# Optimization experiments

Hardware: AMD Instinct MI355X
Metric: run time of the kernel (lower is better)

## Reference

```python
import jax, jax.numpy as jnp
import numpy as np

B, N, D, H, DH, DFF = 2, 2048, 1024, 16, 64, 4096
EPS = 1e-5  # F.layer_norm default


def setup_inputs() -> dict:
    key = jax.random.key(0)
    ks = jax.random.split(key, 8)
    w = lambda k, shape: jax.random.normal(k, shape, dtype=jnp.float32) * 0.02
    # standard rotary frequencies over full head dim (rot_dim = DH)
    inv_freq = 1.0 / (10000.0 ** (jnp.arange(0, DH, 2, dtype=jnp.float32) / DH))
    t = jnp.arange(N, dtype=jnp.float32)
    f = t[:, None] * inv_freq[None, :]          # [N, DH/2]
    freqs = jnp.concatenate([f, f], axis=-1)    # [N, DH]
    return {
        "x": jax.random.normal(ks[0], (B, N, D), dtype=jnp.float32),
        "gamma_pre": jnp.ones((D,), jnp.float32),
        "w_qkv": w(ks[1], (3 * D, D)),
        "w_o": w(ks[2], (D, D)),
        "gamma_ff": jnp.ones((D,), jnp.float32),
        "w_up": w(ks[3], (DFF, D)),
        "b_up": jnp.zeros((DFF,), jnp.float32),
        "w_gate": w(ks[4], (DFF, D)),
        "b_gate": jnp.zeros((DFF,), jnp.float32),
        "w_out": w(ks[5], (D, DFF)),
        "b_out": jnp.zeros((D,), jnp.float32),
        "freqs": freqs,
        "mask": jnp.ones((B, N), dtype=bool),
    }


def _layernorm(x, gamma):
    mu = jnp.mean(x, axis=-1, keepdims=True)
    var = jnp.var(x, axis=-1, keepdims=True)
    return (x - mu) * jax.lax.rsqrt(var + EPS) * gamma


def _rotate_half(x):
    x1, x2 = jnp.split(x, 2, axis=-1)
    return jnp.concatenate([-x2, x1], axis=-1)


def _rope(t, freqs):
    # rot_dim == DH so nothing is left unrotated
    return t * jnp.cos(freqs) + _rotate_half(t) * jnp.sin(freqs)


def reference(x, gamma_pre, w_qkv, w_o, gamma_ff, w_up, b_up, w_gate, b_gate,
              w_out, b_out, freqs, mask):
    b, n, d = x.shape
    # ---- self-attention branch (pre-norm) ----
    h = _layernorm(x, gamma_pre)
    qkv = h @ w_qkv.T                                   # [b, n, 3d]
    q, k, v = jnp.split(qkv, 3, axis=-1)
    to_heads = lambda t: t.reshape(b, n, H, DH).transpose(0, 2, 1, 3)  # b h n d
    q, k, v = to_heads(q), to_heads(k), to_heads(v)
    q = _rope(q, freqs)
    k = _rope(k, freqs)
    scale = 1.0 / np.sqrt(DH).astype(np.float32)
    dots = jnp.einsum('bhid,bhjd->bhij', q, k) * scale  # [b, H, n, n]
    neg = -jnp.finfo(dots.dtype).max
    dots = jnp.where(mask[:, None, None, :], dots, neg)        # key padding mask
    causal = jnp.triu(jnp.ones((n, n), dtype=bool), 1)
    dots = jnp.where(causal, neg, dots)
    attn = jax.nn.softmax(dots.astype(jnp.float32), axis=-1).astype(dots.dtype)
    o = jnp.einsum('bhij,bhjd->bhid', attn, v)
    o = o.transpose(0, 2, 1, 3).reshape(b, n, d) @ w_o.T
    o = jnp.where(mask[..., None], o, 0.0)
    x = x + o
    # ---- GLU feed-forward branch (pre-norm) ----
    h2 = _layernorm(x, gamma_ff)
    up = h2 @ w_up.T + b_up
    gate = h2 @ w_gate.T + b_gate
    ff = (up * jax.nn.silu(gate)) @ w_out.T + b_out
    return x + ff
```

## Files before the change

### kernel.cpp

```cpp
#include <hip/hip_runtime.h>
#include <stdint.h>


#define B_ 2
#define N_ 2048
#define D_ 1024
#define H_ 16
#define DFF_ 4096
#define ROWS_ (B_*N_)

typedef unsigned short u16;
typedef short short4_ __attribute__((ext_vector_type(4)));
typedef short short8 __attribute__((ext_vector_type(8)));
typedef float float4_ __attribute__((ext_vector_type(4)));

#define NEGBIG (-1e30f)
#define QSCALE 0.1803368801111204f

__device__ __forceinline__ float b2f(u16 u) {
  union { unsigned u; float f; } c; c.u = ((unsigned)u) << 16; return c.f;
}
__device__ __forceinline__ u16 f2b(float f) {
  union { float f; unsigned u; } c; c.f = f;
  unsigned x = c.u;
  x += 0x7fffu + ((x >> 16) & 1u);
  return (u16)(x >> 16);
}

__device__ __forceinline__ void gl_lds16(const u16* g, u16* l) {
  __builtin_amdgcn_global_load_lds(
      (const __attribute__((address_space(1))) unsigned int*)g,
      (__attribute__((address_space(3))) unsigned int*)l, 16, 0, 0);
}

__global__ __launch_bounds__(256) void cvt_all(const float* __restrict__ s_qkv,
                                               const float* __restrict__ s_o,
                                               const float* __restrict__ s_up,
                                               const float* __restrict__ s_gate,
                                               const float* __restrict__ s_out,
                                               u16* __restrict__ d_qkv,
                                               u16* __restrict__ d_o,
                                               u16* __restrict__ d_up,
                                               u16* __restrict__ d_gate,
                                               u16* __restrict__ d_out_) {
  int c = blockIdx.x * 256 + threadIdx.x;
  const float* src; u16* dst; int off;
  if (c < 393216)       { src = s_qkv;  dst = d_qkv;  off = c; }
  else if (c < 524288)  { src = s_o;    dst = d_o;    off = c - 393216; }
  else if (c < 1048576) { src = s_up;   dst = d_up;   off = c - 524288; }
  else if (c < 1572864) { src = s_gate; dst = d_gate; off = c - 1048576; }
  else                  { src = s_out;  dst = d_out_; off = c - 1572864; }
  int i = off * 8;
  float4_ v0 = *(const float4_*)(src + i);
  float4_ v1 = *(const float4_*)(src + i + 4);
  short8 pk;
#pragma unroll
  for (int e = 0; e < 4; e++) { pk[e] = (short)f2b(v0[e]); pk[4 + e] = (short)f2b(v1[e]); }
  *(short8*)(dst + i) = pk;
}

__global__ __launch_bounds__(256) void ln_kernel(const float* __restrict__ xin,
                                                 const float* __restrict__ gamma,
                                                 u16* __restrict__ out) {
  int row = blockIdx.x, t = threadIdx.x;
  float4_ v = *(const float4_*)(xin + (size_t)row * D_ + t * 4);
  float s = 0.f, ss = 0.f;
#pragma unroll
  for (int i = 0; i < 4; i++) { s += v[i]; ss += v[i] * v[i]; }
#pragma unroll
  for (int off = 1; off < 64; off <<= 1) {
    s  += __shfl_xor(s, off, 64);
    ss += __shfl_xor(ss, off, 64);
  }
  __shared__ float red[8];
  if ((t & 63) == 0) { red[t >> 6] = s; red[4 + (t >> 6)] = ss; }
  __syncthreads();
  s  = red[0] + red[1] + red[2] + red[3];
  ss = red[4] + red[5] + red[6] + red[7];
  float mu  = s * (1.f / D_);
  float var = ss * (1.f / D_) - mu * mu;
  float rs  = rsqrtf(var + 1e-5f);
#pragma unroll
  for (int i = 0; i < 4; i++)
    out[(size_t)row * D_ + t * 4 + i] = f2b((v[i] - mu) * rs * gamma[t * 4 + i]);
}

__global__ __launch_bounds__(256) void combine_ln(const u16* p0,
                                                  const u16* __restrict__ p1,
                                                  const float* __restrict__ resid,
                                                  const float* __restrict__ gamma,
                                                  float* __restrict__ x1,
                                                  u16* h2out) {
  int row = blockIdx.x, t = threadIdx.x;
  size_t base = (size_t)row * D_ + t * 4;
  short4_ a = *(const short4_*)(p0 + base);
  short4_ b = *(const short4_*)(p1 + base);
  float4_ rv = *(const float4_*)(resid + base);
  float4_ v;
  float s = 0.f, ss = 0.f;
#pragma unroll
  for (int i = 0; i < 4; i++) {
    v[i] = b2f((u16)a[i]) + b2f((u16)b[i]) + rv[i];
    s += v[i]; ss += v[i] * v[i];
  }
  *(float4_*)(x1 + base) = v;
#pragma unroll
  for (int off = 1; off < 64; off <<= 1) {
    s  += __shfl_xor(s, off, 64);
    ss += __shfl_xor(ss, off, 64);
  }
  __shared__ float red[8];
  if ((t & 63) == 0) { red[t >> 6] = s; red[4 + (t >> 6)] = ss; }
  __syncthreads();
  s  = red[0] + red[1] + red[2] + red[3];
  ss = red[4] + red[5] + red[6] + red[7];
  float mu  = s * (1.f / D_);
  float var = ss * (1.f / D_) - mu * mu;
  float rs  = rsqrtf(var + 1e-5f);
#pragma unroll
  for (int i = 0; i < 4; i++)
    h2out[base + i] = f2b((v[i] - mu) * rs * gamma[t * 4 + i]);
}

template <int MODE>
__device__ __forceinline__ void gemm_epilogue(float4_ (&acc)[4][4], void* Cout,
                                              const float* bias, const void* extra,
                                              int mbase, int nbase, int N,
                                              int wr, int wc, int quad, int l16) {
#pragma unroll
  for (int i = 0; i < 4; i++) {
#pragma unroll
    for (int r = 0; r < 4; r++) {
      int row = mbase + wr * 64 + i * 16 + quad * 4 + r;
#pragma unroll
      for (int j = 0; j < 4; j++) {
        int col = nbase + wc * 64 + j * 16 + l16;
        size_t idx = (size_t)row * N + col;
        float v = acc[i][j][r];
        if (MODE == 0) {
          ((u16*)Cout)[idx] = f2b(v);
        } else if (MODE == 1) {
          ((u16*)Cout)[idx] = f2b(v + bias[col]);
        } else if (MODE == 2) {
          ((float*)Cout)[idx] = v + ((const float*)extra)[idx];
        } else if (MODE == 3) {
          float gate = v + bias[col];
          float sig = 1.f / (1.f + expf(-gate));
          float upv = b2f(((const u16*)extra)[idx]);
          ((u16*)Cout)[idx] = f2b(upv * gate * sig);
        } else {
          ((float*)Cout)[idx] = v + bias[col] + ((const float*)extra)[idx];
        }
      }
    }
  }
}

__device__ __forceinline__ void gemm_core64(const u16* A, const u16* W,
                                            float4_ (&acc)[4][4], u16* sA, u16* sW,
                                            int mbase, int nbase, int K,
                                            int klo, int khi,
                                            int wave, int lane, int wr, int wc,
                                            int quad, int l16) {
  int colb = ((lane & 3) ^ ((lane >> 3) & 3)) << 3;
  int qs8  = (quad ^ ((l16 >> 1) & 3)) * 8;
  for (int k0 = klo; k0 < khi; k0 += 64) {
    __syncthreads();
#pragma unroll
    for (int hh = 0; hh < 2; hh++) {
      int kh = k0 + hh * 32;
#pragma unroll
      for (int it = 0; it < 2; it++) {
        int c = wave * 128 + it * 64 + lane;
        int row = c >> 2;
        gl_lds16(A + (size_t)(mbase + row) * K + kh + colb,
                 sA + hh * 4096 + (size_t)(wave * 128 + it * 64) * 8);
        gl_lds16(W + (size_t)(nbase + row) * K + kh + colb,
                 sW + hh * 4096 + (size_t)(wave * 128 + it * 64) * 8);
      }
    }
    __syncthreads();
#pragma unroll
    for (int hh = 0; hh < 2; hh++) {
      const u16* sAp = sA + hh * 4096;
      const u16* sWp = sW + hh * 4096;
      short8 af[4], bf[4];
#pragma unroll
      for (int i = 0; i < 4; i++)
        af[i] = *(const short8*)(sAp + (wr * 64 + i * 16 + l16) * 32 + qs8);
#pragma unroll
      for (int j = 0; j < 4; j++)
        bf[j] = *(const short8*)(sWp + (wc * 64 + j * 16 + l16) * 32 + qs8);
#pragma unroll
      for (int i = 0; i < 4; i++)
#pragma unroll
        for (int j = 0; j < 4; j++)
          acc[i][j] = __builtin_amdgcn_mfma_f32_16x16x32_bf16(af[i], bf[j], acc[i][j], 0, 0, 0);
    }
  }
}

__global__ __launch_bounds__(256) void gemm_bb(const u16* __restrict__ A,
                                               const u16* __restrict__ W,
                                               u16* __restrict__ C,
                                               int M, int N, int K) {
  __shared__ __align__(16) u16 sA[2][128 * 32];
  __shared__ __align__(16) u16 sW[2][128 * 32];
  int t = threadIdx.x;
  int mbase = blockIdx.y * 128, nbase = blockIdx.x * 128;
  int wave = t >> 6, lane = t & 63;
  int wr = wave >> 1, wc = wave & 1;
  int quad = lane >> 4, l16 = lane & 15;

  float4_ z4 = {0.f, 0.f, 0.f, 0.f};
  float4_ acc[4][4];
#pragma unroll
  for (int i = 0; i < 4; i++)
#pragma unroll
    for (int j = 0; j < 4; j++) acc[i][j] = z4;

  gemm_core64(A, W, acc, &sA[0][0], &sW[0][0], mbase, nbase, K,
              0, K, wave, lane, wr, wc, quad, l16);

#pragma unroll
  for (int i = 0; i < 4; i++)
#pragma unroll
    for (int r = 0; r < 4; r++) {
      int row = mbase + wr * 64 + i * 16 + quad * 4 + r;
#pragma unroll
      for (int j = 0; j < 4; j++) {
        int col = nbase + wc * 64 + j * 16 + l16;
        C[(size_t)row * N + col] = f2b(acc[i][j][r]);
      }
    }
}

__global__ __launch_bounds__(256) void gemm_bb_split(const u16* __restrict__ A,
                                                     const u16* __restrict__ W,
                                                     u16* __restrict__ p0,
                                                     u16* __restrict__ p1,
                                                     int M, int N, int K) {
  __shared__ __align__(16) u16 sA[2][128 * 32];
  __shared__ __align__(16) u16 sW[2][128 * 32];
  int t = threadIdx.x;
  int mbase = blockIdx.y * 128, nbase = blockIdx.x * 128;
  int z = blockIdx.z;
  int wave = t >> 6, lane = t & 63;
  int wr = wave >> 1, wc = wave & 1;
  int quad = lane >> 4, l16 = lane & 15;
  int Kh = K >> 1;

  float4_ z4 = {0.f, 0.f, 0.f, 0.f};
  float4_ acc[4][4];
#pragma unroll
  for (int i = 0; i < 4; i++)
#pragma unroll
    for (int j = 0; j < 4; j++) acc[i][j] = z4;

  gemm_core64(A, W, acc, &sA[0][0], &sW[0][0], mbase, nbase, K,
              z * Kh, z * Kh + Kh, wave, lane, wr, wc, quad, l16);

  u16* P = z ? p1 : p0;
#pragma unroll
  for (int i = 0; i < 4; i++)
#pragma unroll
    for (int r = 0; r < 4; r++) {
      int row = mbase + wr * 64 + i * 16 + quad * 4 + r;
#pragma unroll
      for (int j = 0; j < 4; j++) {
        int col = nbase + wc * 64 + j * 16 + l16;
        P[(size_t)row * N + col] = f2b(acc[i][j][r]);
      }
    }
}

__device__ __forceinline__ void glu8_stageA(const u16* A, u16* aslot, int mbase,
                                            int kk, int wave, int lane, int colb) {
  int rw = wave * 16 + (lane >> 2);
#pragma unroll
  for (int it = 0; it < 2; it++) {
    int row = it * 128 + rw;
    gl_lds16(A + (size_t)(mbase + row) * 1024 + kk * 32 + colb,
             aslot + it * 4096 + wave * 512);
  }
}
__device__ __forceinline__ void glu8_stageB(const u16* Wu, const u16* Wg, u16* bslot,
                                            int nbase, int kk, int wave, int lane,
                                            int colb) {
  int rw = wave * 16 + (lane >> 2);
  size_t go = (size_t)(nbase + rw) * 1024 + kk * 32 + colb;
  gl_lds16(Wu + go, bslot + wave * 512);
  gl_lds16(Wg + go, bslot + 4096 + wave * 512);
}

__global__ __launch_bounds__(512) void gemm_glu8(const u16* __restrict__ A,
                                                 const u16* __restrict__ Wu,
                                                 const u16* __restrict__ Wg,
                                                 const float* __restrict__ bu,
                                                 const float* __restrict__ bg,
                                                 u16* __restrict__ G) {
  __shared__ __align__(16) u16 ring[4][16384];
  const int NT = 32;
  int t_ = threadIdx.x, wave = t_ >> 6, lane = t_ & 63;
  int wr = wave >> 2, wc = wave & 3;
  int quad = lane >> 4, l16 = lane & 15;
  int mbase = blockIdx.y * 256, nbase = blockIdx.x * 128;
  int colb = ((lane & 3) ^ ((lane >> 3) & 3)) << 3;
  int qs8  = (quad ^ ((l16 >> 1) & 3)) * 8;

  float4_ z4 = {0.f, 0.f, 0.f, 0.f};
  float4_ acc[8][4];
#pragma unroll
  for (int i = 0; i < 8; i++)
#pragma unroll
    for (int j = 0; j < 4; j++) acc[i][j] = z4;

#pragma unroll
  for (int kk = 0; kk < 3; kk++) {
    glu8_stageA(A, ring[kk], mbase, kk, wave, lane, colb);
    glu8_stageB(Wu, Wg, ring[kk] + 8192, nbase, kk, wave, lane, colb);
  }

  for (int t = 0; t < NT; t++) {
    if (t < NT - 2)       asm volatile("s_waitcnt vmcnt(8)" ::: "memory");
    else if (t == NT - 2) asm volatile("s_waitcnt vmcnt(4)" ::: "memory");
    else                  asm volatile("s_waitcnt vmcnt(0)" ::: "memory");
    __builtin_amdgcn_s_barrier();
    asm volatile("" ::: "memory");

    const u16* as = ring[t & 3];
    const u16* bs = as + 8192;
    bool prefetch = (t + 3 < NT);
    int kk = t + 3;

    if (prefetch) glu8_stageA(A, ring[kk & 3], mbase, kk, wave, lane, colb);
    short8 af[4], bf[4];
#pragma unroll
    for (int i = 0; i < 4; i++)
      af[i] = *(const short8*)(as + (wr * 128 + i * 16 + l16) * 32 + qs8);
#pragma unroll
    for (int j = 0; j < 4; j++)
      bf[j] = *(const short8*)(bs + (wc * 64 + j * 16 + l16) * 32 + qs8);
    __builtin_amdgcn_s_setprio(1);
#pragma unroll
    for (int i = 0; i < 4; i++)
#pragma unroll
      for (int j = 0; j < 4; j++)
        acc[i][j] = __builtin_amdgcn_mfma_f32_16x16x32_bf16(af[i], bf[j], acc[i][j], 0, 0, 0);
    __builtin_amdgcn_s_setprio(0);
    __builtin_amdgcn_s_barrier();
    asm volatile("" ::: "memory");

    if (prefetch) glu8_stageB(Wu, Wg, ring[kk & 3] + 8192, nbase, kk, wave, lane, colb);
    short8 ag[4];
#pragma unroll
    for (int i = 0; i < 4; i++)
      ag[i] = *(const short8*)(as + (wr * 128 + (4 + i) * 16 + l16) * 32 + qs8);
    __builtin_amdgcn_s_setprio(1);
#pragma unroll
    for (int i = 0; i < 4; i++)
#pragma unroll
      for (int j = 0; j < 4; j++)
        acc[4 + i][j] = __builtin_amdgcn_mfma_f32_16x16x32_bf16(ag[i], bf[j], acc[4 + i][j], 0, 0, 0);
    __builtin_amdgcn_s_setprio(0);
  }

  __syncthreads();
  u16* ex = &ring[0][0];
  if (wc >= 2) {
    int cc = (wc - 2) * 64;
#pragma unroll
    for (int i = 0; i < 8; i++)
#pragma unroll
      for (int r = 0; r < 4; r++) {
        int row = wr * 128 + i * 16 + quad * 4 + r;
#pragma unroll
        for (int j = 0; j < 4; j++) {
          int col = cc + j * 16 + l16;
          float gv = acc[i][j][r] + bg[nbase + col];
          float sig = 1.f / (1.f + expf(-gv));
          ex[row * 128 + col] = f2b(gv * sig);
        }
      }
  }
  __syncthreads();
  if (wc < 2) {
    int cc = wc * 64;
#pragma unroll
    for (int i = 0; i < 8; i++)
#pragma unroll
      for (int r = 0; r < 4; r++) {
        int row = wr * 128 + i * 16 + quad * 4 + r;
#pragma unroll
        for (int j = 0; j < 4; j++) {
          int col = cc + j * 16 + l16;
          float uv = acc[i][j][r] + bu[nbase + col];
          G[(size_t)(mbase + row) * DFF_ + nbase + col] =
              f2b(uv * b2f(ex[row * 128 + col]));
        }
      }
  }
}

__global__ __launch_bounds__(256) void split_combine(const u16* __restrict__ p0,
                                                     const u16* __restrict__ p1,
                                                     const float* __restrict__ bias,
                                                     const float* __restrict__ resid,
                                                     float* __restrict__ out, int N) {
  int idx = (blockIdx.x * 256 + threadIdx.x) * 8;
  int col = idx & (N - 1);
  short8 a = *(const short8*)(p0 + idx);
  short8 b = *(const short8*)(p1 + idx);
  float4_ r0 = *(const float4_*)(resid + idx);
  float4_ r1 = *(const float4_*)(resid + idx + 4);
  float4_ o0, o1;
#pragma unroll
  for (int e = 0; e < 4; e++) {
    float bb0 = bias ? bias[col + e] : 0.f;
    float bb1 = bias ? bias[col + 4 + e] : 0.f;
    o0[e] = b2f((u16)a[e]) + b2f((u16)b[e]) + bb0 + r0[e];
    o1[e] = b2f((u16)a[4 + e]) + b2f((u16)b[4 + e]) + bb1 + r1[e];
  }
  *(float4_*)(out + idx) = o0;
  *(float4_*)(out + idx + 4) = o1;
}

template <int MODE>
__global__ __launch_bounds__(256) void gemm_nt(const u16* __restrict__ A,
                                               const float* __restrict__ W,
                                               void* Cout,
                                               const float* __restrict__ bias,
                                               const void* extra,
                                               int M, int N, int K) {
  __shared__ __align__(16) u16 sA[128 * 32];
  __shared__ __align__(16) u16 sW[128 * 32];
  int t = threadIdx.x;
  int mbase = blockIdx.y * 128, nbase = blockIdx.x * 128;
  int wave = t >> 6, lane = t & 63;
  int wr = wave >> 1, wc = wave & 1;
  int quad = lane >> 4, l16 = lane & 15;

  float4_ z4 = {0.f, 0.f, 0.f, 0.f};
  float4_ acc[4][4];
#pragma unroll
  for (int i = 0; i < 4; i++)
#pragma unroll
    for (int j = 0; j < 4; j++) acc[i][j] = z4;

  for (int k0 = 0; k0 < K; k0 += 32) {
    __syncthreads();
#pragma unroll
    for (int it = 0; it < 2; it++) {
      int c = t + 256 * it;
      int row = c >> 2, col = (c & 3) << 3;
      ((short8*)sA)[c] = *(const short8*)(A + (size_t)(mbase + row) * K + k0 + col);
      const float* wp = W + (size_t)(nbase + row) * K + k0 + col;
      float4_ w0 = *(const float4_*)wp;
      float4_ w1 = *(const float4_*)(wp + 4);
      short8 pk;
#pragma unroll
      for (int e = 0; e < 4; e++) { pk[e] = (short)f2b(w0[e]); pk[4 + e] = (short)f2b(w1[e]); }
      ((short8*)sW)[c] = pk;
    }
    __syncthreads();
    short8 af[4], bf[4];
#pragma unroll
    for (int i = 0; i < 4; i++)
      af[i] = *(const short8*)(sA + (wr * 64 + i * 16 + l16) * 32 + quad * 8);
#pragma unroll
    for (int j = 0; j < 4; j++)
      bf[j] = *(const short8*)(sW + (wc * 64 + j * 16 + l16) * 32 + quad * 8);
#pragma unroll
    for (int i = 0; i < 4; i++)
#pragma unroll
      for (int j = 0; j < 4; j++)
        acc[i][j] = __builtin_amdgcn_mfma_f32_16x16x32_bf16(af[i], bf[j], acc[i][j], 0, 0, 0);
  }
  gemm_epilogue<MODE>(acc, Cout, bias, extra, mbase, nbase, N, wr, wc, quad, l16);
}

template <int SPLIT>
__global__ __launch_bounds__(256) void rope_kernel(const u16* __restrict__ q0,
                                                   const u16* __restrict__ q1,
                                                   const float* __restrict__ freqs,
                                                   u16* __restrict__ qr,
                                                   u16* __restrict__ kr,
                                                   u16* __restrict__ vt) {
  int idx = blockIdx.x * 256 + threadIdx.x;
  int d2 = idx & 31;
  int h  = (idx >> 5) & 15;
  int n  = (idx >> 9) & 2047;
  int b  = idx >> 20;
  float f = freqs[n * 64 + d2];
  float c = cosf(f), s = sinf(f);
  size_t base = (size_t)(b * N_ + n) * 3072;
  int hd = h * 64 + d2;
#define LD(o) (SPLIT ? (b2f(q0[base + (o)]) + b2f(q1[base + (o)])) : b2f(q0[base + (o)]))
  float v_q1 = LD(hd),        v_q2 = LD(hd + 32);
  float v_k1 = LD(1024 + hd), v_k2 = LD(1024 + hd + 32);
  float v_v1 = LD(2048 + hd), v_v2 = LD(2048 + hd + 32);
#undef LD
  size_t ro = ((size_t)(b * H_ + h) * N_ + n) * 64 + d2;
  qr[ro]      = f2b((v_q1 * c - v_q2 * s) * QSCALE);
  qr[ro + 32] = f2b((v_q2 * c + v_q1 * s) * QSCALE);
  kr[ro]      = f2b(v_k1 * c - v_k2 * s);
  kr[ro + 32] = f2b(v_k2 * c + v_k1 * s);
  size_t vo = ((size_t)(b * H_ + h) * 64 + d2) * N_ + n;
  vt[vo]           = f2b(v_v1);
  vt[vo + 32 * N_] = f2b(v_v2);
}

#define LP 72
#define NSPLIT 4
__global__ __launch_bounds__(256) void attn_kernel(const u16* __restrict__ qr,
                                                   const u16* __restrict__ kr,
                                                   const u16* __restrict__ vt,
                                                   u16* __restrict__ opart,
                                                   float* __restrict__ mlp) {
  __shared__ __align__(16) u16 sK[64 * LP];
  __shared__ __align__(16) u16 sV[64 * LP];
  __shared__ __align__(16) u16 sP[4][16 * LP];
  int qp = blockIdx.x, bh = blockIdx.y, sp = blockIdx.z;
  int t = threadIdx.x, wave = t >> 6, lane = t & 63;
  int quad = lane >> 4, l16 = lane & 15;
  const u16* qptr = qr + (size_t)bh * N_ * 64;
  const u16* kp = kr + (size_t)bh * N_ * 64;
  const u16* vp = vt + (size_t)bh * 64 * N_;
  float4_ z4 = {0.f, 0.f, 0.f, 0.f};
  short8 onesv;
#pragma unroll
  for (int e = 0; e < 8; e++) onesv[e] = (short)0x3F80;

  for (int qsel = 0; qsel < 2; qsel++) {
    int qt = qsel ? (N_ / 64 - 1 - qp) : qp;
    int qbase = qt * 64;
    int ntiles = qt + 1;
    int ktlo = (ntiles * sp) / NSPLIT, kthi = (ntiles * (sp + 1)) / NSPLIT;

    short8 aq[2];
    int qrow = qbase + wave * 16 + l16;
#pragma unroll
    for (int kk = 0; kk < 2; kk++)
      aq[kk] = *(const short8*)(qptr + (size_t)qrow * 64 + kk * 32 + quad * 8);

    float4_ o[4] = {z4, z4, z4, z4};
    float m_r[4] = {NEGBIG, NEGBIG, NEGBIG, NEGBIG};
    float l_r[4] = {0.f, 0.f, 0.f, 0.f};

    for (int kt = ktlo; kt < kthi; kt++) {
      __syncthreads();
      {
        const u16* src = kp + (size_t)kt * 64 * 64;
#pragma unroll
        for (int it = 0; it < 2; it++) {
          int c = t + 256 * it;
          int row = c >> 3, seg = c & 7;
          *(short8*)(sK + row * LP + seg * 8) = *(const short8*)(src + c * 8);
          *(short8*)(sV + row * LP + seg * 8) =
              *(const short8*)(vp + (size_t)row * N_ + kt * 64 + seg * 8);
        }
      }
      __syncthreads();

      float4_ sf[4];
#pragma unroll
      for (int j = 0; j < 4; j++) {
        short8 bk0 = *(const short8*)(sK + (j * 16 + l16) * LP + quad * 8);
        short8 bk1 = *(const short8*)(sK + (j * 16 + l16) * LP + 32 + quad * 8);
        float4_ acc = z4;
        acc = __builtin_amdgcn_mfma_f32_16x16x32_bf16(aq[0], bk0, acc, 0, 0, 0);
        acc = __builtin_amdgcn_mfma_f32_16x16x32_bf16(aq[1], bk1, acc, 0, 0, 0);
        sf[j] = acc;
      }
      if (kt == qt) {
#pragma unroll
        for (int j = 0; j < 4; j++)
#pragma unroll
          for (int r = 0; r < 4; r++) {
            int ig = qbase + wave * 16 + quad * 4 + r;
            int jg = kt * 64 + j * 16 + l16;
            if (jg > ig) sf[j][r] = NEGBIG;
          }
      }

      float alpha_r[4], mt_r[4];
#pragma unroll
      for (int r = 0; r < 4; r++)
        mt_r[r] = fmaxf(fmaxf(sf[0][r], sf[1][r]), fmaxf(sf[2][r], sf[3][r]));
      bool need = (mt_r[0] > m_r[0] + 8.f) || (mt_r[1] > m_r[1] + 8.f) ||
                  (mt_r[2] > m_r[2] + 8.f) || (mt_r[3] > m_r[3] + 8.f);
      if (__any(need)) {
#pragma unroll
        for (int r = 0; r < 4; r++) {
          float mt = mt_r[r];
#pragma unroll
          for (int off = 1; off < 16; off <<= 1) mt = fmaxf(mt, __shfl_xor(mt, off, 64));
          float mn = fmaxf(m_r[r], mt);
          alpha_r[r] = exp2f(m_r[r] - mn);
          m_r[r] = mn;
#pragma unroll
          for (int jo = 0; jo < 4; jo++) o[jo][r] *= alpha_r[r];
        }
      } else {
#pragma unroll
        for (int r = 0; r < 4; r++) alpha_r[r] = 1.f;
      }
#pragma unroll
      for (int r = 0; r < 4; r++)
#pragma unroll
        for (int j = 0; j < 4; j++) sf[j][r] = exp2f(sf[j][r] - m_r[r]);

      u16* sPw = sP[wave];
#pragma unroll
      for (int j = 0; j < 4; j++)
#pragma unroll
        for (int r = 0; r < 4; r++)
          sPw[(quad * 4 + r) * LP + j * 16 + l16] = f2b(sf[j][r]);
      short8 ap[2];
#pragma unroll
      for (int kk = 0; kk < 2; kk++)
        ap[kk] = *(const short8*)(sPw + l16 * LP + kk * 32 + quad * 8);

      float4_ ls = z4;
      ls = __builtin_amdgcn_mfma_f32_16x16x32_bf16(ap[0], onesv, ls, 0, 0, 0);
      ls = __builtin_amdgcn_mfma_f32_16x16x32_bf16(ap[1], onesv, ls, 0, 0, 0);
#pragma unroll
      for (int r = 0; r < 4; r++) l_r[r] = l_r[r] * alpha_r[r] + ls[r];

#pragma unroll
      for (int jo = 0; jo < 4; jo++)
#pragma unroll
        for (int kk = 0; kk < 2; kk++) {
          short8 bv = *(const short8*)(sV + (jo * 16 + l16) * LP + kk * 32 + quad * 8);
          o[jo] = __builtin_amdgcn_mfma_f32_16x16x32_bf16(ap[kk], bv, o[jo], 0, 0, 0);
        }
    }

#pragma unroll
    for (int r = 0; r < 4; r++) {
      int n = qbase + wave * 16 + quad * 4 + r;
      size_t row = (size_t)bh * N_ + n;
      if (l16 == 0) {
        mlp[2 * (sp * (size_t)65536 + row)]     = m_r[r];
        mlp[2 * (sp * (size_t)65536 + row) + 1] = l_r[r];
      }
#pragma unroll
      for (int jo = 0; jo < 4; jo++)
        opart[sp * (size_t)4194304 + row * 64 + jo * 16 + l16] = f2b(o[jo][r]);
    }
  }
}

__global__ __launch_bounds__(256) void attn_combine(const u16* __restrict__ opart,
                                                    const float* __restrict__ mlp,
                                                    u16* __restrict__ obuf) {
  int idx = blockIdx.x * 256 + threadIdx.x;
  int row = idx >> 3, seg = idx & 7;
  float mm[NSPLIT], ll[NSPLIT];
  float mmax = NEGBIG;
#pragma unroll
  for (int s = 0; s < NSPLIT; s++) {
    mm[s] = mlp[2 * (s * (size_t)65536 + row)];
    ll[s] = mlp[2 * (s * (size_t)65536 + row) + 1];
    mmax = fmaxf(mmax, mm[s]);
  }
  float w[NSPLIT], lsum = 0.f;
#pragma unroll
  for (int s = 0; s < NSPLIT; s++) { w[s] = exp2f(mm[s] - mmax); lsum += ll[s] * w[s]; }
  float inv = 1.f / lsum;
  float acc[8] = {0, 0, 0, 0, 0, 0, 0, 0};
#pragma unroll
  for (int s = 0; s < NSPLIT; s++) {
    short8 a = *(const short8*)(opart + s * (size_t)4194304 + (size_t)row * 64 + seg * 8);
#pragma unroll
    for (int e = 0; e < 8; e++) acc[e] += b2f((u16)a[e]) * w[s];
  }
  short8 r;
#pragma unroll
  for (int e = 0; e < 8; e++) r[e] = (short)f2b(acc[e] * inv);
  int bh = row >> 11, n = row & 2047;
  int bb = bh >> 4, h = bh & 15;
  *(short8*)(obuf + ((size_t)(bb * N_ + n) * D_) + h * 64 + seg * 8) = r;
}

extern "C" void kernel_launch(void* const* d_in, const int* in_sizes, int n_in,
                              void* d_out, int out_size, void* d_ws, size_t ws_size,
                              hipStream_t stream) {
  const float* x         = (const float*)d_in[0];
  const float* gamma_pre = (const float*)d_in[1];
  const float* w_qkv     = (const float*)d_in[2];
  const float* w_o       = (const float*)d_in[3];
  const float* gamma_ff  = (const float*)d_in[4];
  const float* w_up      = (const float*)d_in[5];
  const float* b_up      = (const float*)d_in[6];
  const float* w_gate    = (const float*)d_in[7];
  const float* b_gate    = (const float*)d_in[8];
  const float* w_out     = (const float*)d_in[9];
  const float* b_out     = (const float*)d_in[10];
  const float* freqs     = (const float*)d_in[11];

  char* ws = (char*)d_ws;
  const size_t MB = 1024 * 1024;
  float* out = (float*)d_out;
  bool wide = ws_size >= 96 * MB;

  if (wide) {
    u16*  h     = (u16*)(ws);
    u16*  qkv   = (u16*)(ws + 8 * MB);
    u16*  qr    = (u16*)(ws + 56 * MB);
    u16*  kr    = (u16*)d_out;
    u16*  vtb   = (u16*)d_out + 4194304;
    u16*  opart = (u16*)(ws);
    float* mlb  = (float*)(ws + 32 * MB);
    u16*  ob    = (u16*)(ws + 34 * MB);
    u16*  sp0   = (u16*)(ws);
    u16*  sp1o  = (u16*)(ws + 8 * MB);
    float* x1   = (float*)(ws + 16 * MB);
    u16*  h2    = (u16*)(ws);
    u16*  g     = (u16*)(ws + 32 * MB);
    u16*  sp0f  = (u16*)(ws);
    u16*  sp1f  = (u16*)(ws + 8 * MB);
    u16* wb_qkv  = (u16*)(ws + 64 * MB);
    u16* wb_o    = (u16*)(ws + 70 * MB);
    u16* wb_up   = (u16*)(ws + 72 * MB);
    u16* wb_gate = (u16*)(ws + 80 * MB);
    u16* wb_out  = (u16*)(ws + 88 * MB);

    cvt_all<<<8192, 256, 0, stream>>>(w_qkv, w_o, w_up, w_gate, w_out,
                                      wb_qkv, wb_o, wb_up, wb_gate, wb_out);
    ln_kernel<<<ROWS_, 256, 0, stream>>>(x, gamma_pre, h);
    gemm_bb<<<dim3(3072 / 128, ROWS_ / 128), 256, 0, stream>>>(
        h, wb_qkv, qkv, ROWS_, 3072, 1024);
    rope_kernel<0><<<(B_ * N_ * H_ * 32) / 256, 256, 0, stream>>>(
        qkv, qkv, freqs, qr, kr, vtb);
    attn_kernel<<<dim3(N_ / 128, B_ * H_, NSPLIT), 256, 0, stream>>>(
        qr, kr, vtb, opart, mlb);
    attn_combine<<<(B_ * H_ * N_ * 8) / 256, 256, 0, stream>>>(opart, mlb, ob);
    gemm_bb_split<<<dim3(1024 / 128, ROWS_ / 128, 2), 256, 0, stream>>>(
        ob, wb_o, sp0, sp1o, ROWS_, 1024, 1024);
    combine_ln<<<ROWS_, 256, 0, stream>>>(sp0, sp1o, x, gamma_ff, x1, h2);
    gemm_glu8<<<dim3(DFF_ / 128, ROWS_ / 256), 512, 0, stream>>>(
        h2, wb_up, wb_gate, b_up, b_gate, g);
    gemm_bb_split<<<dim3(1024 / 128, ROWS_ / 128, 2), 256, 0, stream>>>(
        g, wb_out, sp0f, sp1f, ROWS_, 1024, 4096);
    split_combine<<<(ROWS_ * 1024) / 2048, 256, 0, stream>>>(
        sp0f, sp1f, b_out, x1, out, 1024);
  } else {
    u16*  h     = (u16*)(ws);
    u16*  qkv   = (u16*)(ws + 8 * MB);
    u16*  qr    = (u16*)(ws + 32 * MB);
    u16*  kr    = (u16*)(ws + 40 * MB);
    u16*  vtb   = (u16*)(ws + 48 * MB);
    u16*  ob    = (u16*)(ws + 56 * MB);
    float* x1   = (float*)(ws + 8 * MB);
    u16*  h2    = (u16*)(ws + 24 * MB);
    u16*  g     = (u16*)(ws + 32 * MB);

    ln_kernel<<<ROWS_, 256, 0, stream>>>(x, gamma_pre, h);
    gemm_nt<0><<<dim3(3072 / 128, ROWS_ / 128), 256, 0, stream>>>(
        h, w_qkv, qkv, nullptr, nullptr, ROWS_, 3072, 1024);
    rope_kernel<0><<<(B_ * N_ * H_ * 32) / 256, 256, 0, stream>>>(
        qkv, qkv, freqs, qr, kr, vtb);
    attn_kernel<<<dim3(N_ / 128, B_ * H_, NSPLIT), 256, 0, stream>>>(
        qr, kr, vtb, (u16*)(ws), (float*)(ws + 32 * MB));
    attn_combine<<<(B_ * H_ * N_ * 8) / 256, 256, 0, stream>>>(
        (u16*)(ws), (float*)(ws + 32 * MB), ob);
    gemm_nt<2><<<dim3(1024 / 128, ROWS_ / 128), 256, 0, stream>>>(
        ob, w_o, x1, nullptr, x, ROWS_, 1024, 1024);
    ln_kernel<<<ROWS_, 256, 0, stream>>>(x1, gamma_ff, h2);
    gemm_nt<1><<<dim3(4096 / 128, ROWS_ / 128), 256, 0, stream>>>(
        h2, w_up, g, b_up, nullptr, ROWS_, 4096, 1024);
    gemm_nt<3><<<dim3(4096 / 128, ROWS_ / 128), 256, 0, stream>>>(
        h2, w_gate, g, b_gate, g, ROWS_, 4096, 1024);
    gemm_nt<4><<<dim3(1024 / 128, ROWS_ / 128), 256, 0, stream>>>(
        g, w_out, (void*)out, b_out, x1, ROWS_, 1024, 4096);
  }
}
```

Measured before the change: 450.2 us.

## Switch GLU GEMM from 4-slot ring to double-buffered LDS pipeline

Replaces the GLU GEMM's 4-slot LDS ring (3-deep prefetch, split A/B staging between two MFMA halves) with a 2-slot double buffer that prefetches only the next K-tile before computing the current one in a single MFMA block. This halves LDS usage (64KB vs 128KB) so more blocks can be resident per CU, and it simplifies the wait counts. The cost is a shallower prefetch, so global-load latency has less time to hide. It also loads all 8 A fragments at once, which raises register pressure.

```diff
diff --git a/kernel.cpp b/kernel.cpp
--- a/kernel.cpp
+++ b/kernel.cpp
@@ -274,23 +274,19 @@
     }
 }
 
-__device__ __forceinline__ void glu8_stageA(const u16* A, u16* aslot, int mbase,
-                                            int kk, int wave, int lane, int colb) {
+__device__ __forceinline__ void glu8_stage(const u16* A, const u16* Wu,
+                                           const u16* Wg, u16* sl, int mbase,
+                                           int nbase, int kk, int wave, int lane,
+                                           int colb) {
   int rw = wave * 16 + (lane >> 2);
-#pragma unroll
-  for (int it = 0; it < 2; it++) {
-    int row = it * 128 + rw;
-    gl_lds16(A + (size_t)(mbase + row) * 1024 + kk * 32 + colb,
-             aslot + it * 4096 + wave * 512);
-  }
-}
-__device__ __forceinline__ void glu8_stageB(const u16* Wu, const u16* Wg, u16* bslot,
-                                            int nbase, int kk, int wave, int lane,
-                                            int colb) {
-  int rw = wave * 16 + (lane >> 2);
-  size_t go = (size_t)(nbase + rw) * 1024 + kk * 32 + colb;
-  gl_lds16(Wu + go, bslot + wave * 512);
-  gl_lds16(Wg + go, bslot + 4096 + wave * 512);
+  int kc = kk * 32 + colb;
+#pragma unroll
+  for (int it = 0; it < 2; it++)
+    gl_lds16(A + (size_t)(mbase + it * 128 + rw) * 1024 + kc,
+             sl + it * 4096 + wave * 512);
+  size_t go = (size_t)(nbase + rw) * 1024 + kc;
+  gl_lds16(Wu + go, sl + 8192 + wave * 512);
+  gl_lds16(Wg + go, sl + 12288 + wave * 512);
 }
 
 __global__ __launch_bounds__(512) void gemm_glu8(const u16* __restrict__ A,
@@ -299,7 +295,7 @@
                                                  const float* __restrict__ bu,
                                                  const float* __restrict__ bg,
                                                  u16* __restrict__ G) {
-  __shared__ __align__(16) u16 ring[4][16384];
+  __shared__ __align__(16) u16 ring[2][16384];
   const int NT = 32;
   int t_ = threadIdx.x, wave = t_ >> 6, lane = t_ & 63;
   int wr = wave >> 2, wc = wave & 3;
@@ -315,54 +311,37 @@
 #pragma unroll
     for (int j = 0; j < 4; j++) acc[i][j] = z4;
 
-#pragma unroll
-  for (int kk = 0; kk < 3; kk++) {
-    glu8_stageA(A, ring[kk], mbase, kk, wave, lane, colb);
-    glu8_stageB(Wu, Wg, ring[kk] + 8192, nbase, kk, wave, lane, colb);
-  }
+  glu8_stage(A, Wu, Wg, &ring[0][0], mbase, nbase, 0, wave, lane, colb);
 
   for (int t = 0; t < NT; t++) {
-    if (t < NT - 2)       asm volatile("s_waitcnt vmcnt(8)" ::: "memory");
-    else if (t == NT - 2) asm volatile("s_waitcnt vmcnt(4)" ::: "memory");
-    else                  asm volatile("s_waitcnt vmcnt(0)" ::: "memory");
+    if (t + 1 < NT) {
+      glu8_stage(A, Wu, Wg, &ring[(t + 1) & 1][0], mbase, nbase, t + 1,
+                 wave, lane, colb);
+      asm volatile("s_waitcnt vmcnt(4)" ::: "memory");
+    } else {
+      asm volatile("s_waitcnt vmcnt(0)" ::: "memory");
+    }
     __builtin_amdgcn_s_barrier();
     asm volatile("" ::: "memory");
 
-    const u16* as = ring[t & 3];
+    const u16* as = ring[t & 1];
     const u16* bs = as + 8192;
-    bool prefetch = (t + 3 < NT);
-    int kk = t + 3;
-
-    if (prefetch) glu8_stageA(A, ring[kk & 3], mbase, kk, wave, lane, colb);
-    short8 af[4], bf[4];
-#pragma unroll
-    for (int i = 0; i < 4; i++)
+    short8 af[8], bf[4];
+#pragma unroll
+    for (int i = 0; i < 8; i++)
       af[i] = *(const short8*)(as + (wr * 128 + i * 16 + l16) * 32 + qs8);
 #pragma unroll
     for (int j = 0; j < 4; j++)
       bf[j] = *(const short8*)(bs + (wc * 64 + j * 16 + l16) * 32 + qs8);
     __builtin_amdgcn_s_setprio(1);
 #pragma unroll
-    for (int i = 0; i < 4; i++)
+    for (int i = 0; i < 8; i++)
 #pragma unroll
       for (int j = 0; j < 4; j++)
         acc[i][j] = __builtin_amdgcn_mfma_f32_16x16x32_bf16(af[i], bf[j], acc[i][j], 0, 0, 0);
     __builtin_amdgcn_s_setprio(0);
     __builtin_amdgcn_s_barrier();
     asm volatile("" ::: "memory");
-
-    if (prefetch) glu8_stageB(Wu, Wg, ring[kk & 3] + 8192, nbase, kk, wave, lane, colb);
-    short8 ag[4];
-#pragma unroll
-    for (int i = 0; i < 4; i++)
-      ag[i] = *(const short8*)(as + (wr * 128 + (4 + i) * 16 + l16) * 32 + qs8);
-    __builtin_amdgcn_s_setprio(1);
-#pragma unroll
-    for (int i = 0; i < 4; i++)
-#pragma unroll
-      for (int j = 0; j < 4; j++)
-        acc[4 + i][j] = __builtin_amdgcn_mfma_f32_16x16x32_bf16(ag[i], bf[j], acc[4 + i][j], 0, 0, 0);
-    __builtin_amdgcn_s_setprio(0);
   }
 
   __syncthreads();
```

New measurement: 437.5 us. -2.8%, faster.
